# Kernel tuning notes

Hardware: AMD Instinct MI355X
Metric: run time of the kernel (lower is better)

## Reference

```python
import jax, jax.numpy as jnp
import numpy as np

N_DRUG, N_DIS = 3072, 3072
N = N_DRUG + N_DIS
E = 196608
F1, F2, F3 = 512, 256, 128
GAMMA1 = GAMMA2 = GAMMA3 = 0.03125
NEG_SLOPE = 0.2   # GATConv default negative_slope
KERNEL_W = 0.25   # drug_ps/dis_ps = 1/kernel_len


def gat_layer(x, src, dst, w_e, W, a_src, a_dst, b):
    """Single-head GATConv: gather -> per-node softmax -> scatter-aggregate.
    Edge weights w_e scale the unnormalized attention."""
    xw = x @ W                                                  # [N, F]
    e = jax.nn.leaky_relu((xw @ a_src)[src] + (xw @ a_dst)[dst], NEG_SLOPE)  # [E]
    m = jax.ops.segment_max(e, dst, num_segments=N)
    ex = jnp.exp(e - m[dst]) * w_e
    denom = jax.ops.segment_sum(ex, dst, num_segments=N)
    alpha = ex / (denom[dst] + 1e-16)
    out = jax.ops.segment_sum(alpha[:, None] * xw[src], dst, num_segments=N)
    return out + b


def gip_kernel(y, gamma):
    """getGipKernel(y, 0, gamma, normalized=True)."""
    mn = jnp.min(y, axis=1, keepdims=True)
    mx = jnp.max(y, axis=1, keepdims=True)
    y = (y - mn) / (mx - mn + 1e-12)          # row-wise min-max normalize
    k = y @ y.T
    k = k / jnp.mean(jnp.diagonal(k))
    d = jnp.diagonal(k)
    dist = d[:, None] + d[None, :] - 2.0 * k  # kernelToDistance
    return jnp.exp(-gamma * dist)


def normalized_kernel(K):
    K = jnp.abs(K)
    minv = jnp.min(jnp.where(K > 0, K, jnp.inf))
    K = jnp.where(K == 0, minv, K)            # replace zeros with min nonzero
    d = jnp.sqrt(jnp.diagonal(K))
    return K / (d[:, None] * d[None, :])


def setup_inputs() -> dict:
    key = jax.random.key(0)
    ks = jax.random.split(key, 20)
    f32 = jnp.float32

    def lin(k, fi, fo):
        return jax.random.normal(k, (fi, fo), f32) * (1.0 / float(np.sqrt(fi)))

    inp = {
        'x': jax.random.normal(ks[0], (N, N), f32),
        'edge_index': jax.random.randint(ks[1], (2, E), 0, N, dtype=jnp.int32),
        'adj_data': jax.random.uniform(ks[2], (N, N), f32),
        'drug_sim': jax.random.uniform(ks[3], (N_DRUG, N_DRUG), f32),
        'dis_sim': jax.random.uniform(ks[4], (N_DIS, N_DIS), f32),
        'alpha1': jax.random.normal(ks[5], (N_DRUG, N_DIS), f32),
        'alpha2': jax.random.normal(ks[6], (N_DIS, N_DRUG), f32),
        'W1': lin(ks[7], N, F1),
        'as1': jax.random.normal(ks[8], (F1,), f32) * 0.1,
        'ad1': jax.random.normal(ks[9], (F1,), f32) * 0.1,
        'b1': jnp.zeros((F1,), f32),
        'W2': lin(ks[10], F1, F2),
        'as2': jax.random.normal(ks[11], (F2,), f32) * 0.1,
        'ad2': jax.random.normal(ks[12], (F2,), f32) * 0.1,
        'b2': jnp.zeros((F2,), f32),
        'W3': lin(ks[13], F2, F3),
        'as3': jax.random.normal(ks[14], (F3,), f32) * 0.1,
        'ad3': jax.random.normal(ks[15], (F3,), f32) * 0.1,
        'b3': jnp.zeros((F3,), f32),
    }
    return inp


def reference(x, edge_index, adj_data, drug_sim, dis_sim, alpha1, alpha2,
              W1, as1, ad1, b1, W2, as2, ad2, b2, W3, as3, ad3, b3):
    src0, dst0 = edge_index[0], edge_index[1]
    w0 = adj_data[src0, dst0]                  # per-edge gather of dense weights
    loop = jnp.arange(N, dtype=src0.dtype)     # GATConv add_self_loops=True
    src = jnp.concatenate([src0, loop])
    dst = jnp.concatenate([dst0, loop])
    w = jnp.concatenate([w0, jnp.ones((N,), adj_data.dtype)])

    H1 = jax.nn.relu(gat_layer(x, src, dst, w, W1, as1, ad1, b1))
    H2 = jax.nn.relu(gat_layer(H1, src, dst, w, W2, as2, ad2, b2))
    H3 = jax.nn.relu(gat_layer(H2, src, dst, w, W3, as3, ad3, b3))

    drug_k = KERNEL_W * (gip_kernel(H1[:N_DRUG], GAMMA1)
                         + gip_kernel(H2[:N_DRUG], GAMMA2)
                         + gip_kernel(H3[:N_DRUG], GAMMA3) + drug_sim)
    dis_k = KERNEL_W * (gip_kernel(H1[N_DRUG:], GAMMA1)
                        + gip_kernel(H2[N_DRUG:], GAMMA2)
                        + gip_kernel(H3[N_DRUG:], GAMMA3) + dis_sim)

    out1 = normalized_kernel(drug_k) @ alpha1  # [N_DRUG, N_DIS]
    out2 = normalized_kernel(dis_k) @ alpha2   # [N_DIS, N_DRUG]
    return 0.5 * (out1 + out2.T)
```

## Files before the change

### kernel.cpp

```cpp
#include <hip/hip_runtime.h>
#include <hip/hip_bf16.h>
#include <stdint.h>

#define N_NODES 6144
#define N_DRUG  3072
#define N_EDGE  196608
#define E_TOT   (N_EDGE + N_NODES)
#define GAMMA   0.03125f

typedef __bf16 bf16x8 __attribute__((ext_vector_type(8)));
typedef float  f32x4  __attribute__((ext_vector_type(4)));

__device__ __forceinline__ unsigned short f2b(float f){
  union { float f; unsigned u; } v; v.f = f;
  unsigned r = v.u + 0x7FFFu + ((v.u >> 16) & 1u);
  return (unsigned short)(r >> 16);
}
__device__ __forceinline__ float b2f(unsigned short b){
  union { unsigned u; float f; } v; v.u = ((unsigned)b) << 16;
  return v.f;
}
__device__ __forceinline__ void gl_lds(const void* g, void* l){
  __builtin_amdgcn_global_load_lds((const __attribute__((address_space(1))) void*)g,
                                   (__attribute__((address_space(3))) void*)l, 16, 0, 0);
}

#define WAITVM(N) asm volatile("s_waitcnt vmcnt(" #N ")" ::: "memory")
#define SYNC() { __builtin_amdgcn_sched_barrier(0); __builtin_amdgcn_s_barrier(); __builtin_amdgcn_sched_barrier(0); }

__global__ void cast_bf16_k(const float* __restrict__ in, unsigned short* __restrict__ out, long n){
  long i = ((long)blockIdx.x*blockDim.x + threadIdx.x)*4;
  long stride = (long)gridDim.x*blockDim.x*4;
  for (; i < n; i += stride){
    float4 v = *(const float4*)(in + i);
    ushort4 o;
    o.x = f2b(v.x); o.y = f2b(v.y); o.z = f2b(v.z); o.w = f2b(v.w);
    *(ushort4*)(out + i) = o;
  }
}

__global__ void tcast_k(const float* __restrict__ in, unsigned short* __restrict__ out,
                        int R, int Cd, int OLD, int OOFF){
  __shared__ float tile[32][33];
  int bx = blockIdx.x*32, by = blockIdx.y*32;
  int tx = threadIdx.x, ty = threadIdx.y;
  for (int i = ty; i < 32; i += 8) tile[i][tx] = in[(long)(by+i)*Cd + bx + tx];
  __syncthreads();
  for (int i = ty; i < 32; i += 8) out[(long)(bx+i)*OLD + OOFF + by + tx] = f2b(tile[tx][i]);
}

__global__ void tcast2_k(const float* __restrict__ a2, const float* __restrict__ a1,
                         unsigned short* __restrict__ o0, unsigned short* __restrict__ o1){
  __shared__ float tile[32][33];
  const float* in = blockIdx.z ? a1 : a2;
  unsigned short* out = blockIdx.z ? o1 : o0;
  int OOFF = blockIdx.z ? 0 : N_DRUG;
  int bx = blockIdx.x*32, by = blockIdx.y*32;
  int tx = threadIdx.x, ty = threadIdx.y;
  for (int i = ty; i < 32; i += 8) tile[i][tx] = in[(long)(by+i)*N_DRUG + bx + tx];
  __syncthreads();
  for (int i = ty; i < 32; i += 8) out[(long)(bx+i)*N_NODES + OOFF + by + tx] = f2b(tile[tx][i]);
}

__global__ void hist_k(const int* __restrict__ ei, int* __restrict__ cnt){
  int i = blockIdx.x*blockDim.x + threadIdx.x;
  if (i >= E_TOT) return;
  int d = (i < N_EDGE) ? ei[N_EDGE + i] : (i - N_EDGE);
  atomicAdd(&cnt[d], 1);
}

__global__ void scan_k(const int* __restrict__ cnt, int* __restrict__ ptr){
  __shared__ int sums[1024];
  int t = threadIdx.x;
  int v[6]; int s = 0;
  #pragma unroll
  for (int i = 0; i < 6; i++){ v[i] = s; s += cnt[t*6 + i]; }
  sums[t] = s; __syncthreads();
  for (int off = 1; off < 1024; off <<= 1){
    int add = (t >= off) ? sums[t - off] : 0;
    __syncthreads();
    sums[t] += add;
    __syncthreads();
  }
  int base = (t == 0) ? 0 : sums[t-1];
  #pragma unroll
  for (int i = 0; i < 6; i++) ptr[t*6 + i] = base + v[i];
  if (t == 1023) ptr[N_NODES] = sums[1023];
}

__global__ void scatter_k(const int* __restrict__ ei, const int* __restrict__ ptr,
                          int* __restrict__ cur, int* __restrict__ srcs,
                          int* __restrict__ epos){
  int i = blockIdx.x*blockDim.x + threadIdx.x;
  if (i >= E_TOT) return;
  int s = (i < N_EDGE) ? ei[i] : (i - N_EDGE);
  int d = (i < N_EDGE) ? ei[N_EDGE + i] : (i - N_EDGE);
  int pos = ptr[d] + atomicAdd(&cur[d], 1);
  srcs[pos] = s; epos[i] = pos;
}

__global__ void dots_k(const float* __restrict__ XW, const float* __restrict__ av,
                       const float* __restrict__ dv, float* __restrict__ es,
                       float* __restrict__ ed, float* __restrict__ denom, int F){
  int n = blockIdx.x, l = threadIdx.x;
  float s = 0.f, d = 0.f;
  for (int f = l; f < F; f += 64){
    float x = XW[(long)n*F + f];
    s += x * av[f]; d += x * dv[f];
  }
  #pragma unroll
  for (int off = 32; off > 0; off >>= 1){ s += __shfl_down(s, off); d += __shfl_down(d, off); }
  if (l == 0){ es[n] = s; ed[n] = d; denom[n] = 0.f; }
}

__global__ void phase12_k(const int* __restrict__ ei, const float* __restrict__ adj,
                          const float* __restrict__ es, const float* __restrict__ ed,
                          const int* __restrict__ epos, float* __restrict__ exc,
                          float* __restrict__ denom){
  int i = blockIdx.x*blockDim.x + threadIdx.x;
  if (i >= E_TOT) return;
  int s = (i < N_EDGE) ? ei[i] : (i - N_EDGE);
  int d = (i < N_EDGE) ? ei[N_EDGE + i] : (i - N_EDGE);
  float w = (i < N_EDGE) ? adj[(long)s*N_NODES + d] : 1.0f;
  float e = es[s] + ed[d];
  e = (e > 0.f) ? e : 0.2f*e;
  float ex = expf(e) * w;
  exc[epos[i]] = ex;
  atomicAdd(&denom[d], ex);
}

__global__ void agg4_k(const unsigned short* __restrict__ XWb, const int* __restrict__ ptr,
                       const int* __restrict__ srcs, const float* __restrict__ exc,
                       const float* __restrict__ denom, const float* __restrict__ bias,
                       float* __restrict__ H, unsigned short* __restrict__ Hb, int F){
  int n = blockIdx.x, t = threadIdx.x;
  int st = ptr[n], en = ptr[n+1];
  float a0v = 0.f, a1v = 0.f, a2v = 0.f, a3v = 0.f;
  int j = st;
  for (; j + 1 < en; j += 2){
    float w0 = exc[j], w1 = exc[j+1];
    int s0 = srcs[j], s1 = srcs[j+1];
    ushort4 u0 = *(const ushort4*)(XWb + (long)s0*F + t*4);
    ushort4 u1 = *(const ushort4*)(XWb + (long)s1*F + t*4);
    a0v += w0*b2f(u0.x) + w1*b2f(u1.x); a1v += w0*b2f(u0.y) + w1*b2f(u1.y);
    a2v += w0*b2f(u0.z) + w1*b2f(u1.z); a3v += w0*b2f(u0.w) + w1*b2f(u1.w);
  }
  if (j < en){
    float w0 = exc[j]; int s0 = srcs[j];
    ushort4 u0 = *(const ushort4*)(XWb + (long)s0*F + t*4);
    a0v += w0*b2f(u0.x); a1v += w0*b2f(u0.y); a2v += w0*b2f(u0.z); a3v += w0*b2f(u0.w);
  }
  float invd = 1.f/(denom[n] + 1e-16f);
  float4 b = *(const float4*)(bias + t*4);
  float4 o;
  o.x = fmaxf(a0v*invd + b.x, 0.f); o.y = fmaxf(a1v*invd + b.y, 0.f);
  o.z = fmaxf(a2v*invd + b.z, 0.f); o.w = fmaxf(a3v*invd + b.w, 0.f);
  *(float4*)(H + (long)n*F + t*4) = o;
  if (Hb){
    ushort4 ob; ob.x = f2b(o.x); ob.y = f2b(o.y); ob.z = f2b(o.z); ob.w = f2b(o.w);
    *(ushort4*)(Hb + (long)n*F + t*4) = ob;
  }
}

__global__ void agg_k(const unsigned short* __restrict__ XWb, const int* __restrict__ ptr,
                      const int* __restrict__ srcs, const float* __restrict__ exc,
                      const float* __restrict__ denom, const float* __restrict__ bias,
                      float* __restrict__ H, unsigned short* __restrict__ Hb, int F){
  int n = blockIdx.x, t = threadIdx.x;
  int st = ptr[n], en = ptr[n+1];
  float ax = 0.f, ay = 0.f;
  int j = st;
  for (; j + 1 < en; j += 2){
    float a0 = exc[j], a1 = exc[j+1];
    int s0 = srcs[j], s1 = srcs[j+1];
    ushort2 u0 = *(const ushort2*)(XWb + (long)s0*F + t*2);
    ushort2 u1 = *(const ushort2*)(XWb + (long)s1*F + t*2);
    ax += a0*b2f(u0.x) + a1*b2f(u1.x);
    ay += a0*b2f(u0.y) + a1*b2f(u1.y);
  }
  if (j < en){
    float a = exc[j]; int s = srcs[j];
    ushort2 u = *(const ushort2*)(XWb + (long)s*F + t*2);
    ax += a*b2f(u.x); ay += a*b2f(u.y);
  }
  float invd = 1.f/(denom[n] + 1e-16f);
  float2 b = *(const float2*)(bias + t*2);
  float vx = fmaxf(ax*invd + b.x, 0.f);
  float vy = fmaxf(ay*invd + b.y, 0.f);
  *(float2*)(H + (long)n*F + t*2) = make_float2(vx, vy);
  if (Hb){
    ushort2 o; o.x = f2b(vx); o.y = f2b(vy);
    *(ushort2*)(Hb + (long)n*F + t*2) = o;
  }
}

__global__ void rownorm_all_k(const float* __restrict__ H0, const float* __restrict__ H1,
                              const float* __restrict__ H2,
                              unsigned short* __restrict__ y0, unsigned short* __restrict__ y1,
                              float* __restrict__ dv0, float* __restrict__ dv1){
  int seg = blockIdx.y;
  int side = seg / 3, layer = seg % 3;
  int F = 512 >> layer;
  const float* H = (layer == 0) ? H0 : (layer == 1) ? H1 : H2;
  H += (size_t)(side ? N_DRUG : 0) * F;
  unsigned short* yb = ((side ? y1 : y0) + ((layer == 0) ? 0 : (layer == 1) ? 512 : 768));
  float* dvec = (side ? dv1 : dv0) + layer*N_DRUG;

  int r = blockIdx.x, t = threadIdx.x;
  __shared__ float ra[256], rb[256];
  float mn = 3.4e38f, mx = -3.4e38f;
  for (int f = t; f < F; f += 256){
    float v = H[(long)r*F + f];
    mn = fminf(mn, v); mx = fmaxf(mx, v);
  }
  ra[t] = mn; rb[t] = mx; __syncthreads();
  for (int s2 = 128; s2 > 0; s2 >>= 1){
    if (t < s2){ ra[t] = fminf(ra[t], ra[t+s2]); rb[t] = fmaxf(rb[t], rb[t+s2]); }
    __syncthreads();
  }
  mn = ra[0]; mx = rb[0];
  __syncthreads();
  float sc = 1.f/(mx - mn + 1e-12f);
  float s = 0.f;
  for (int f = t; f < F; f += 256){
    float v = (H[(long)r*F + f] - mn)*sc;
    unsigned short b = f2b(v);
    yb[(long)r*896 + f] = b;
    float vb = b2f(b);
    s += vb*vb;
  }
  ra[t] = s; __syncthreads();
  for (int s2 = 128; s2 > 0; s2 >>= 1){
    if (t < s2) ra[t] += ra[t+s2];
    __syncthreads();
  }
  if (t == 0) dvec[r] = ra[0];
}

__global__ void vsum_diag_k(const float* __restrict__ dv0, const float* __restrict__ dv1,
                            float* __restrict__ sump,
                            const float* __restrict__ sim0, const float* __restrict__ sim1,
                            float* __restrict__ rs0, float* __restrict__ rs1){
  int y = blockIdx.y;
  int t = threadIdx.x;
  if (y < 6){
    int side = y / 3, layer = y % 3;
    const float* v = (side ? dv1 : dv0) + layer*N_DRUG;
    __shared__ float red[256];
    float s = 0.f;
    for (int i = blockIdx.x*256 + t; i < N_DRUG; i += gridDim.x*256) s += v[i];
    red[t] = s; __syncthreads();
    for (int s2 = 128; s2 > 0; s2 >>= 1){ if (t < s2) red[t] += red[t+s2]; __syncthreads(); }
    if (t == 0) atomicAdd(&sump[y], red[0]);
  } else {
    int side = y - 6;
    int i = blockIdx.x*256 + t;
    const float* sim = side ? sim1 : sim0;
    float* rs = side ? rs1 : rs0;
    if (i < N_DRUG) rs[i] = rsqrtf(sim[(long)i*N_DRUG + i] + 3.0f);
  }
}

__global__ __launch_bounds__(512, 2) void gemm8p(
    const unsigned short* __restrict__ A, const unsigned short* __restrict__ Bt,
    float* __restrict__ P, float* __restrict__ Palt, int M, int N, int K, int kz)
{
  __shared__ unsigned short lds[2][2][16384];
  int t = threadIdx.x;
  int lane = t & 63, wave = t >> 6;
  int wm = wave >> 2, wn = wave & 3;

  int nbx = gridDim.x;
  int nwg = nbx * gridDim.y;
  int bid = blockIdx.y * nbx + blockIdx.x;
  int cpx = nwg >> 3;
  int swz = (bid & 7) * cpx + (bid >> 3);
  long brow = (long)(swz / nbx) * 256;
  long bcol = (long)(swz % nbx) * 256;
  long k0 = (long)blockIdx.z * kz;
  int nt = kz >> 6;

  int sr = wave*8 + (lane >> 3);
  int cg = (lane & 7) ^ (lane >> 3);
  const unsigned short* gA = A  + (brow + sr)*(long)K + k0 + cg*8;
  const unsigned short* gB = Bt + (bcol + sr)*(long)K + k0 + cg*8;
  unsigned ldsw = wave * 512;

  auto stage = [&](int b, int mat, int h, int tk){
    const unsigned short* g = (mat ? gB : gA) + (long)(h*128)*K + (long)tk*64;
    unsigned short* d = &lds[b][mat][h*8192 + ldsw];
    gl_lds(g, d);
    gl_lds(g + (long)64*K, d + 4096);
  };

  int fr = lane & 15, q = lane >> 4;
  int lo = fr*64 + ((q ^ (fr & 7))*8);
  int dk = (lo ^ 32) - lo;

  f32x4 acc[8][4];
  #pragma unroll
  for (int a = 0; a < 8; a++)
    #pragma unroll
    for (int b = 0; b < 4; b++){ acc[a][b][0]=0.f; acc[a][b][1]=0.f; acc[a][b][2]=0.f; acc[a][b][3]=0.f; }
  bf16x8 af[4][2], bf[4][2];

  const unsigned short* a0p = &lds[0][0][wm*8192 + lo];
  const unsigned short* b0p = &lds[0][1][wn*4096 + lo];
  const unsigned short* a1p = &lds[1][0][wm*8192 + lo];
  const unsigned short* b1p = &lds[1][1][wn*4096 + lo];

#define RD_AF_LO(ab) { _Pragma("unroll") for (int j = 0; j < 4; ++j){ \
    af[j][0] = *(const bf16x8*)((ab) + j*1024); af[j][1] = *(const bf16x8*)((ab) + j*1024 + dk); } }
#define RD_AF_HI(ab) { _Pragma("unroll") for (int j = 0; j < 4; ++j){ \
    af[j][0] = *(const bf16x8*)((ab) + (4+j)*1024); af[j][1] = *(const bf16x8*)((ab) + (4+j)*1024 + dk); } }
#define RD_BF_LO(bb) { _Pragma("unroll") for (int j = 0; j < 2; ++j){ \
    bf[j][0] = *(const bf16x8*)((bb) + j*1024); bf[j][1] = *(const bf16x8*)((bb) + j*1024 + dk); } }
#define RD_BF_HI(bb) { _Pragma("unroll") for (int j = 2; j < 4; ++j){ \
    bf[j][0] = *(const bf16x8*)((bb) + j*1024); bf[j][1] = *(const bf16x8*)((bb) + j*1024 + dk); } }
#define MFMA_Q(MB, NB) { __builtin_amdgcn_s_setprio(1); \
    _Pragma("unroll") for (int kk = 0; kk < 2; ++kk) \
      _Pragma("unroll") for (int mi = 0; mi < 4; ++mi) \
        _Pragma("unroll") for (int ni = (NB); ni < (NB)+2; ++ni) \
          acc[(MB)+mi][ni] = __builtin_amdgcn_mfma_f32_16x16x32_bf16(af[mi][kk], bf[ni][kk], acc[(MB)+mi][ni], 0, 0, 0); \
    __builtin_amdgcn_s_setprio(0); }

  stage(0,0,0,0); stage(0,0,1,0); stage(0,1,0,0); stage(0,1,1,0);
  stage(1,1,0,1); stage(1,1,1,1);
  WAITVM(4);
  SYNC();

  int half = nt >> 1;
  for (int i = 0; i < half; ++i){
    int t1 = 2*i+1, t2 = 2*i+2, t3 = 2*i+3;
    bool s2 = t2 < nt, s3 = t3 < nt;
    RD_AF_LO(a0p); RD_BF_LO(b0p);
    stage(1,0,0,t1);
    SYNC(); MFMA_Q(0,0); SYNC();
    RD_BF_HI(b0p);
    stage(1,0,1,t1);
    SYNC(); MFMA_Q(0,2); SYNC();
    RD_AF_HI(a0p);
    if (s2) stage(0,1,0,t2);
    SYNC(); MFMA_Q(4,0); SYNC();
    if (s2){ stage(0,1,1,t2); WAITVM(4); } else { WAITVM(0); }
    SYNC(); MFMA_Q(4,2); SYNC();
    RD_AF_LO(a1p); RD_BF_LO(b1p);
    if (s2) stage(0,0,0,t2);
    SYNC(); MFMA_Q(0,0); SYNC();
    RD_BF_HI(b1p);
    if (s2) stage(0,0,1,t2);
    SYNC(); MFMA_Q(0,2); SYNC();
    RD_AF_HI(a1p);
    if (s3) stage(1,1,0,t3);
    SYNC(); MFMA_Q(4,0); SYNC();
    if (s3){ stage(1,1,1,t3); WAITVM(4); } else { WAITVM(0); }
    SYNC(); MFMA_Q(4,2); SYNC();
  }
#undef RD_AF_LO
#undef RD_AF_HI
#undef RD_BF_LO
#undef RD_BF_HI
#undef MFMA_Q

  int z = blockIdx.z;
  float* Pz = (z < 2) ? (P + (long)z*M*N) : (Palt + (long)(z-2)*M*N);
  #pragma unroll
  for (int mi = 0; mi < 8; ++mi){
    #pragma unroll
    for (int ni = 0; ni < 4; ++ni){
      long col = bcol + wn*64 + ni*16 + fr;
      #pragma unroll
      for (int r = 0; r < 4; ++r){
        long row = brow + wm*128 + mi*16 + q*4 + r;
        Pz[row*N + col] = acc[mi][ni][r];
      }
    }
  }
}

__global__ void reduce4b_k(const float* __restrict__ p, float* __restrict__ out,
                           unsigned short* __restrict__ outb, long n){
  long i = ((long)blockIdx.x*blockDim.x + threadIdx.x)*4;
  if (i >= n) return;
  float4 s = *(const float4*)(p + i);
  #pragma unroll
  for (int z = 1; z < 4; z++){
    float4 x = *(const float4*)(p + (long)z*n + i);
    s.x += x.x; s.y += x.y; s.z += x.z; s.w += x.w;
  }
  *(float4*)(out + i) = s;
  ushort4 o; o.x = f2b(s.x); o.y = f2b(s.y); o.z = f2b(s.z); o.w = f2b(s.w);
  *(ushort4*)(outb + i) = o;
}

__global__ void reduce3h_k(const float* __restrict__ pa, const float* __restrict__ pb,
                           const float* __restrict__ pc, float* __restrict__ out, long n){
  long i = ((long)blockIdx.x*blockDim.x + threadIdx.x)*4;
  if (i >= n) return;
  float4 a = *(const float4*)(pa + i);
  float4 b = *(const float4*)(pb + i);
  float4 c = *(const float4*)(pc + i);
  float4 o;
  o.x = 0.5f*(a.x + b.x + c.x); o.y = 0.5f*(a.y + b.y + c.y);
  o.z = 0.5f*(a.z + b.z + c.z); o.w = 0.5f*(a.w + b.w + c.w);
  *(float4*)(out + i) = o;
}

__global__ __launch_bounds__(256) void gemm_tn(
    const unsigned short* __restrict__ A, const unsigned short* __restrict__ Bt,
    float* __restrict__ C, unsigned short* __restrict__ Cb, int M, int N, int K)
{
  __shared__ unsigned short As[2][128*64];
  __shared__ unsigned short Bs[2][128*64];
  int t = threadIdx.x;
  int wave = t >> 6, lane = t & 63;
  int brow = blockIdx.y*128, bcol = blockIdx.x*128;
  int wr = (wave >> 1)*64, wc = (wave & 1)*64;
  int fr = lane & 15, q = lane >> 4;
  int rin = lane >> 3, kslot = (lane & 7) ^ rin;

  f32x4 acc[4][4];
  #pragma unroll
  for (int a = 0; a < 4; a++)
    #pragma unroll
    for (int b = 0; b < 4; b++){ acc[a][b][0]=0.f; acc[a][b][1]=0.f; acc[a][b][2]=0.f; acc[a][b][3]=0.f; }

  int aoff[4][2], boff[4][2];
  #pragma unroll
  for (int mi = 0; mi < 4; mi++){
    int row = wr + mi*16 + fr;
    #pragma unroll
    for (int kk = 0; kk < 2; kk++) aoff[mi][kk] = row*64 + (((kk*4 + q) ^ (row & 7))*8);
  }
  #pragma unroll
  for (int ni = 0; ni < 4; ni++){
    int row = wc + ni*16 + fr;
    #pragma unroll
    for (int kk = 0; kk < 2; kk++) boff[ni][kk] = row*64 + (((kk*4 + q) ^ (row & 7))*8);
  }

  auto stage = [&](int buf, int k0){
    #pragma unroll
    for (int p = 0; p < 4; p++){
      int rsec = p*32 + wave*8;
      gl_lds(A  + (long)(brow + rsec + rin)*K + k0 + kslot*8, &As[buf][rsec*64]);
      gl_lds(Bt + (long)(bcol + rsec + rin)*K + k0 + kslot*8, &Bs[buf][rsec*64]);
    }
  };

  int nsteps = K >> 6;
  stage(0, 0);
  __syncthreads();
  int curb = 0;
  for (int s = 0; s < nsteps; s++){
    if (s + 1 < nsteps) stage(curb ^ 1, (s + 1)*64);
    const unsigned short* a_l = As[curb];
    const unsigned short* b_l = Bs[curb];
    #pragma unroll
    for (int kk = 0; kk < 2; kk++){
      bf16x8 af[4], bfv[4];
      #pragma unroll
      for (int mi = 0; mi < 4; mi++) af[mi]  = *(const bf16x8*)(a_l + aoff[mi][kk]);
      #pragma unroll
      for (int ni = 0; ni < 4; ni++) bfv[ni] = *(const bf16x8*)(b_l + boff[ni][kk]);
      #pragma unroll
      for (int mi = 0; mi < 4; mi++)
        #pragma unroll
        for (int ni = 0; ni < 4; ni++)
          acc[mi][ni] = __builtin_amdgcn_mfma_f32_16x16x32_bf16(af[mi], bfv[ni], acc[mi][ni], 0, 0, 0);
    }
    __syncthreads();
    curb ^= 1;
  }

  #pragma unroll
  for (int mi = 0; mi < 4; mi++){
    #pragma unroll
    for (int ni = 0; ni < 4; ni++){
      int col = bcol + wc + ni*16 + fr;
      #pragma unroll
      for (int r = 0; r < 4; r++){
        int row = brow + wr + mi*16 + q*4 + r;
        long idx = (long)row*N + col;
        float v = acc[mi][ni][r];
        C[idx] = v;
        if (Cb) Cb[idx] = f2b(v);
      }
    }
  }
}

__global__ __launch_bounds__(512) void gip_gemm(
    const unsigned short* __restrict__ Y0, const unsigned short* __restrict__ Y1,
    const float* __restrict__ sim0, const float* __restrict__ sim1,
    const float* __restrict__ dva, const float* __restrict__ dvb,
    const float* __restrict__ sumps,
    const float* __restrict__ rs0, const float* __restrict__ rs1,
    unsigned short* __restrict__ o0, unsigned short* __restrict__ o1)
{
  __shared__ unsigned short As[2][128*64];
  __shared__ unsigned short Bs[2][128*64];
  const int K = 896;
  int side = blockIdx.z;
  const unsigned short* Y = side ? Y1 : Y0;
  const float* sim  = side ? sim1 : sim0;
  const float* dv   = side ? dvb : dva;
  const float* sums = sumps + side*3;
  const float* rs   = side ? rs1 : rs0;
  unsigned short* outp = side ? o1 : o0;
  int outoff = side ? N_DRUG : 0;

  int t = threadIdx.x;
  int wave = t >> 6, lane = t & 63;
  int brow = blockIdx.y*128, bcol = blockIdx.x*128;
  int wr = (wave >> 1)*32, wc = (wave & 1)*64;
  int fr = lane & 15, q = lane >> 4;
  int rin = lane >> 3, kslot = (lane & 7) ^ rin;

  f32x4 acc0[2][4], acc1[2][4], acc2[2][4];
  #pragma unroll
  for (int a = 0; a < 2; a++)
    #pragma unroll
    for (int b = 0; b < 4; b++){
      acc0[a][b][0]=0.f;acc0[a][b][1]=0.f;acc0[a][b][2]=0.f;acc0[a][b][3]=0.f;
      acc1[a][b][0]=0.f;acc1[a][b][1]=0.f;acc1[a][b][2]=0.f;acc1[a][b][3]=0.f;
      acc2[a][b][0]=0.f;acc2[a][b][1]=0.f;acc2[a][b][2]=0.f;acc2[a][b][3]=0.f;
    }

  int aoff[2][2], boff[4][2];
  #pragma unroll
  for (int mi = 0; mi < 2; mi++){
    int row = wr + mi*16 + fr;
    #pragma unroll
    for (int kk = 0; kk < 2; kk++) aoff[mi][kk] = row*64 + (((kk*4 + q) ^ (row & 7))*8);
  }
  #pragma unroll
  for (int ni = 0; ni < 4; ni++){
    int row = wc + ni*16 + fr;
    #pragma unroll
    for (int kk = 0; kk < 2; kk++) boff[ni][kk] = row*64 + (((kk*4 + q) ^ (row & 7))*8);
  }

  auto stage = [&](int buf, int k0){
    #pragma unroll
    for (int p = 0; p < 2; p++){
      int rsec = p*64 + wave*8;
      gl_lds(Y + (long)(brow + rsec + rin)*K + k0 + kslot*8, &As[buf][rsec*64]);
      gl_lds(Y + (long)(bcol + rsec + rin)*K + k0 + kslot*8, &Bs[buf][rsec*64]);
    }
  };

  int curb = 0, s = 0;
  stage(0, 0);
  __syncthreads();

#define GSTEP(ACC) { \
    if (s + 1 < 14) stage(curb ^ 1, (s + 1)*64); \
    const unsigned short* a_l = As[curb]; \
    const unsigned short* b_l = Bs[curb]; \
    _Pragma("unroll") \
    for (int kk = 0; kk < 2; kk++){ \
      bf16x8 af0 = *(const bf16x8*)(a_l + aoff[0][kk]); \
      bf16x8 af1 = *(const bf16x8*)(a_l + aoff[1][kk]); \
      _Pragma("unroll") \
      for (int ni = 0; ni < 4; ni++){ \
        bf16x8 bv = *(const bf16x8*)(b_l + boff[ni][kk]); \
        ACC[0][ni] = __builtin_amdgcn_mfma_f32_16x16x32_bf16(af0, bv, ACC[0][ni], 0, 0, 0); \
        ACC[1][ni] = __builtin_amdgcn_mfma_f32_16x16x32_bf16(af1, bv, ACC[1][ni], 0, 0, 0); \
      } \
    } \
    __syncthreads(); curb ^= 1; s++; }

  for (int i = 0; i < 8; i++) GSTEP(acc0)
  for (int i = 0; i < 4; i++) GSTEP(acc1)
  for (int i = 0; i < 2; i++) GSTEP(acc2)
#undef GSTEP

  float im0 = (float)N_DRUG / sums[0];
  float im1 = (float)N_DRUG / sums[1];
  float im2 = (float)N_DRUG / sums[2];
  #pragma unroll
  for (int mi = 0; mi < 2; mi++){
    #pragma unroll
    for (int ni = 0; ni < 4; ni++){
      int col = bcol + wc + ni*16 + fr;
      float d0c = dv[col], d1c = dv[N_DRUG + col], d2c = dv[2*N_DRUG + col];
      float rc = rs[col];
      #pragma unroll
      for (int r = 0; r < 4; r++){
        int row = brow + wr + mi*16 + q*4 + r;
        float v = sim[(long)row*N_DRUG + col]
                + expf(-GAMMA*((dv[row]            + d0c - 2.f*acc0[mi][ni][r])*im0))
                + expf(-GAMMA*((dv[N_DRUG + row]   + d1c - 2.f*acc1[mi][ni][r])*im1))
                + expf(-GAMMA*((dv[2*N_DRUG + row] + d2c - 2.f*acc2[mi][ni][r])*im2));
        outp[(long)row*N_NODES + outoff + col] = f2b(v * rs[row] * rc);
      }
    }
  }
}

extern "C" void kernel_launch(void* const* d_in, const int* in_sizes, int n_in,
                              void* d_out, int out_size, void* d_ws, size_t ws_size,
                              hipStream_t stream){
  const float* x        = (const float*)d_in[0];
  const int*   ei       = (const int*)d_in[1];
  const float* adj      = (const float*)d_in[2];
  const float* drug_sim = (const float*)d_in[3];
  const float* dis_sim  = (const float*)d_in[4];
  const float* alpha1   = (const float*)d_in[5];
  const float* alpha2   = (const float*)d_in[6];
  const float* W[3]   = {(const float*)d_in[7],  (const float*)d_in[11], (const float*)d_in[15]};
  const float* as_[3] = {(const float*)d_in[8],  (const float*)d_in[12], (const float*)d_in[16]};
  const float* ad_[3] = {(const float*)d_in[9],  (const float*)d_in[13], (const float*)d_in[17]};
  const float* bs_[3] = {(const float*)d_in[10], (const float*)d_in[14], (const float*)d_in[18]};
  float* out = (float*)d_out;
  const int Fs[3] = {512, 256, 128};

  char* p = (char*)d_ws;
  auto alloc = [&](size_t bytes)->char*{
    char* r = p; p += (bytes + 255) & ~(size_t)255; return r;
  };
  unsigned short* xb  = (unsigned short*)alloc((size_t)N_NODES*N_NODES*2);
  unsigned short* wb  = (unsigned short*)alloc((size_t)N_NODES*512*2);
  float* XW           = (float*)alloc((size_t)N_NODES*512*4);
  unsigned short* XWb = (unsigned short*)alloc((size_t)N_NODES*512*2);
  float* Hf[3];
  Hf[0] = (float*)alloc((size_t)N_NODES*512*4);
  Hf[1] = (float*)alloc((size_t)N_NODES*256*4);
  Hf[2] = (float*)alloc((size_t)N_NODES*128*4);
  unsigned short* Hb  = (unsigned short*)alloc((size_t)N_NODES*512*2);
  float* es    = (float*)alloc(N_NODES*4);
  float* edv   = (float*)alloc(N_NODES*4);
  float* denom = (float*)alloc(N_NODES*4);
  float* exc   = (float*)alloc((size_t)E_TOT*4);
  int* cntcur  = (int*)alloc((size_t)2*N_NODES*4);
  int* cnt = cntcur, *cur = cntcur + N_NODES;
  int* cptr = (int*)alloc((N_NODES+1)*4);
  int* srcs = (int*)alloc((size_t)E_TOT*4);
  int* epos = (int*)alloc((size_t)E_TOT*4);
  unsigned short* ycat[2];
  ycat[0] = (unsigned short*)alloc((size_t)N_DRUG*896*2);
  ycat[1] = (unsigned short*)alloc((size_t)N_DRUG*896*2);
  float* dvv[2];
  dvv[0] = (float*)alloc((size_t)3*N_DRUG*4);
  dvv[1] = (float*)alloc((size_t)3*N_DRUG*4);
  float* sump = (float*)alloc(256);
  float* rsv[2];
  rsv[0] = (float*)alloc(N_DRUG*4);
  rsv[1] = (float*)alloc(N_DRUG*4);
  unsigned short* Abuf  = (unsigned short*)alloc((size_t)N_DRUG*N_NODES*2);
  unsigned short* Btbuf = (unsigned short*)alloc((size_t)N_DRUG*N_NODES*2);

  float* pL1 = (float*)Abuf;
  float* pF01 = (float*)xb;
  float* pF2  = (float*)XW;
  const long MN = (long)N_DRUG*N_DRUG;

  cast_bf16_k<<<4096, 256, 0, stream>>>(x, xb, (long)N_NODES*N_NODES);
  hipMemsetAsync(cntcur, 0, (size_t)2*N_NODES*4, stream);
  hist_k<<<(E_TOT+255)/256, 256, 0, stream>>>(ei, cnt);
  scan_k<<<1, 1024, 0, stream>>>(cnt, cptr);
  scatter_k<<<(E_TOT+255)/256, 256, 0, stream>>>(ei, cptr, cur, srcs, epos);

  const unsigned short* Ain = xb;
  int Kin = N_NODES;
  for (int l = 0; l < 3; l++){
    int F = Fs[l];
    tcast_k<<<dim3(F/32, Kin/32), dim3(32,8), 0, stream>>>(W[l], wb, Kin, F, Kin, 0);
    if (l == 0){
      gemm8p<<<dim3(F/256, N_NODES/256, 4), 512, 0, stream>>>(Ain, wb, pL1, pL1 + 2*(long)N_NODES*F, N_NODES, F, Kin, Kin/4);
      reduce4b_k<<<(int)(((long)N_NODES*F/4 + 255)/256), 256, 0, stream>>>(pL1, XW, XWb, (long)N_NODES*F);
    } else {
      gemm_tn<<<dim3(F/128, N_NODES/128), 256, 0, stream>>>(Ain, wb, XW, XWb, N_NODES, F, Kin);
    }
    dots_k<<<N_NODES, 64, 0, stream>>>(XW, as_[l], ad_[l], es, edv, denom, F);
    phase12_k<<<(E_TOT+255)/256, 256, 0, stream>>>(ei, adj, es, edv, epos, exc, denom);
    unsigned short* HbOut = (l < 2) ? Hb : nullptr;
    if (F >= 256)
      agg4_k<<<N_NODES, F/4, 0, stream>>>(XWb, cptr, srcs, exc, denom, bs_[l], Hf[l], HbOut, F);
    else
      agg_k<<<N_NODES, 64, 0, stream>>>(XWb, cptr, srcs, exc, denom, bs_[l], Hf[l], HbOut, F);
    Ain = Hb; Kin = F;
  }

  hipMemsetAsync(sump, 0, 24, stream);
  rownorm_all_k<<<dim3(N_DRUG, 6), 256, 0, stream>>>(Hf[0], Hf[1], Hf[2],
                                                     ycat[0], ycat[1], dvv[0], dvv[1]);
  vsum_diag_k<<<dim3(12, 8), 256, 0, stream>>>(dvv[0], dvv[1], sump,
                                               drug_sim, dis_sim, rsv[0], rsv[1]);

  tcast2_k<<<dim3(N_DRUG/32, N_DRUG/32, 2), dim3(32,8), 0, stream>>>(alpha2, alpha1, Abuf, Btbuf);

  gip_gemm<<<dim3(N_DRUG/128, N_DRUG/128, 2), 512, 0, stream>>>(
      ycat[0], ycat[1], drug_sim, dis_sim, dvv[0], dvv[1], sump, rsv[0], rsv[1], Abuf, Btbuf);

  gemm8p<<<dim3(N_DRUG/256, N_DRUG/256, 3), 512, 0, stream>>>(Abuf, Btbuf, pF01, pF2, N_DRUG, N_DRUG, N_NODES, N_NODES/3);
  reduce3h_k<<<(int)((MN/4 + 255)/256), 256, 0, stream>>>(pF01, pF01 + MN, pF2, out, MN);

  (void)in_sizes; (void)n_in; (void)out_size; (void)ws_size;
}
```

Before: 600.0 us.

## Drop fp32 activation copies and precompute CSR-ordered edge weights once

Stops writing fp32 copies of XW and the layer outputs and keeps only the bf16 versions, which dots_k and rownorm now read. The per-edge adjacency gather moves into scatter_k, done once into CSR order together with destination indices, so phase12 reads srcs/dsts/wcsr contiguously instead of gathering adj and writing exc through epos every layer. This cuts memory traffic, at the cost of computing the attention logits and min-max normalisation from bf16-rounded values.

Measured after the change: 623.3 us. 3.9% more time.

```diff
diff --git a/kernel.cpp b/kernel.cpp
--- a/kernel.cpp
+++ b/kernel.cpp
@@ -88,24 +88,26 @@
   if (t == 1023) ptr[N_NODES] = sums[1023];
 }
 
-__global__ void scatter_k(const int* __restrict__ ei, const int* __restrict__ ptr,
-                          int* __restrict__ cur, int* __restrict__ srcs,
-                          int* __restrict__ epos){
+__global__ void scatter_k(const int* __restrict__ ei, const float* __restrict__ adj,
+                          const int* __restrict__ ptr, int* __restrict__ cur,
+                          int* __restrict__ srcs, int* __restrict__ dsts,
+                          float* __restrict__ wcsr){
   int i = blockIdx.x*blockDim.x + threadIdx.x;
   if (i >= E_TOT) return;
   int s = (i < N_EDGE) ? ei[i] : (i - N_EDGE);
   int d = (i < N_EDGE) ? ei[N_EDGE + i] : (i - N_EDGE);
   int pos = ptr[d] + atomicAdd(&cur[d], 1);
-  srcs[pos] = s; epos[i] = pos;
-}
-
-__global__ void dots_k(const float* __restrict__ XW, const float* __restrict__ av,
+  srcs[pos] = s; dsts[pos] = d;
+  wcsr[pos] = (i < N_EDGE) ? adj[(long)s*N_NODES + d] : 1.0f;
+}
+
+__global__ void dots_k(const unsigned short* __restrict__ XWb, const float* __restrict__ av,
                        const float* __restrict__ dv, float* __restrict__ es,
                        float* __restrict__ ed, float* __restrict__ denom, int F){
   int n = blockIdx.x, l = threadIdx.x;
   float s = 0.f, d = 0.f;
   for (int f = l; f < F; f += 64){
-    float x = XW[(long)n*F + f];
+    float x = b2f(XWb[(long)n*F + f]);
     s += x * av[f]; d += x * dv[f];
   }
   #pragma unroll
@@ -113,26 +115,24 @@
   if (l == 0){ es[n] = s; ed[n] = d; denom[n] = 0.f; }
 }
 
-__global__ void phase12_k(const int* __restrict__ ei, const float* __restrict__ adj,
+__global__ void phase12_k(const int* __restrict__ srcs, const int* __restrict__ dsts,
+                          const float* __restrict__ wcsr,
                           const float* __restrict__ es, const float* __restrict__ ed,
-                          const int* __restrict__ epos, float* __restrict__ exc,
-                          float* __restrict__ denom){
-  int i = blockIdx.x*blockDim.x + threadIdx.x;
-  if (i >= E_TOT) return;
-  int s = (i < N_EDGE) ? ei[i] : (i - N_EDGE);
-  int d = (i < N_EDGE) ? ei[N_EDGE + i] : (i - N_EDGE);
-  float w = (i < N_EDGE) ? adj[(long)s*N_NODES + d] : 1.0f;
+                          float* __restrict__ exc, float* __restrict__ denom){
+  int p = blockIdx.x*blockDim.x + threadIdx.x;
+  if (p >= E_TOT) return;
+  int s = srcs[p], d = dsts[p];
   float e = es[s] + ed[d];
   e = (e > 0.f) ? e : 0.2f*e;
-  float ex = expf(e) * w;
-  exc[epos[i]] = ex;
+  float ex = expf(e) * wcsr[p];
+  exc[p] = ex;
   atomicAdd(&denom[d], ex);
 }
 
 __global__ void agg4_k(const unsigned short* __restrict__ XWb, const int* __restrict__ ptr,
                        const int* __restrict__ srcs, const float* __restrict__ exc,
                        const float* __restrict__ denom, const float* __restrict__ bias,
-                       float* __restrict__ H, unsigned short* __restrict__ Hb, int F){
+                       unsigned short* __restrict__ Hb, int F){
   int n = blockIdx.x, t = threadIdx.x;
   int st = ptr[n], en = ptr[n+1];
   float a0v = 0.f, a1v = 0.f, a2v = 0.f, a3v = 0.f;
@@ -152,20 +152,16 @@
   }
   float invd = 1.f/(denom[n] + 1e-16f);
   float4 b = *(const float4*)(bias + t*4);
-  float4 o;
-  o.x = fmaxf(a0v*invd + b.x, 0.f); o.y = fmaxf(a1v*invd + b.y, 0.f);
-  o.z = fmaxf(a2v*invd + b.z, 0.f); o.w = fmaxf(a3v*invd + b.w, 0.f);
-  *(float4*)(H + (long)n*F + t*4) = o;
-  if (Hb){
-    ushort4 ob; ob.x = f2b(o.x); ob.y = f2b(o.y); ob.z = f2b(o.z); ob.w = f2b(o.w);
-    *(ushort4*)(Hb + (long)n*F + t*4) = ob;
-  }
+  ushort4 ob;
+  ob.x = f2b(fmaxf(a0v*invd + b.x, 0.f)); ob.y = f2b(fmaxf(a1v*invd + b.y, 0.f));
+  ob.z = f2b(fmaxf(a2v*invd + b.z, 0.f)); ob.w = f2b(fmaxf(a3v*invd + b.w, 0.f));
+  *(ushort4*)(Hb + (long)n*F + t*4) = ob;
 }
 
 __global__ void agg_k(const unsigned short* __restrict__ XWb, const int* __restrict__ ptr,
                       const int* __restrict__ srcs, const float* __restrict__ exc,
                       const float* __restrict__ denom, const float* __restrict__ bias,
-                      float* __restrict__ H, unsigned short* __restrict__ Hb, int F){
+                      unsigned short* __restrict__ Hb, int F){
   int n = blockIdx.x, t = threadIdx.x;
   int st = ptr[n], en = ptr[n+1];
   float ax = 0.f, ay = 0.f;
@@ -185,23 +181,20 @@
   }
   float invd = 1.f/(denom[n] + 1e-16f);
   float2 b = *(const float2*)(bias + t*2);
-  float vx = fmaxf(ax*invd + b.x, 0.f);
-  float vy = fmaxf(ay*invd + b.y, 0.f);
-  *(float2*)(H + (long)n*F + t*2) = make_float2(vx, vy);
-  if (Hb){
-    ushort2 o; o.x = f2b(vx); o.y = f2b(vy);
-    *(ushort2*)(Hb + (long)n*F + t*2) = o;
-  }
-}
-
-__global__ void rownorm_all_k(const float* __restrict__ H0, const float* __restrict__ H1,
-                              const float* __restrict__ H2,
+  ushort2 o;
+  o.x = f2b(fmaxf(ax*invd + b.x, 0.f));
+  o.y = f2b(fmaxf(ay*invd + b.y, 0.f));
+  *(ushort2*)(Hb + (long)n*F + t*2) = o;
+}
+
+__global__ void rownorm_all_k(const unsigned short* __restrict__ H0, const unsigned short* __restrict__ H1,
+                              const unsigned short* __restrict__ H2,
                               unsigned short* __restrict__ y0, unsigned short* __restrict__ y1,
                               float* __restrict__ dv0, float* __restrict__ dv1){
   int seg = blockIdx.y;
   int side = seg / 3, layer = seg % 3;
   int F = 512 >> layer;
-  const float* H = (layer == 0) ? H0 : (layer == 1) ? H1 : H2;
+  const unsigned short* H = (layer == 0) ? H0 : (layer == 1) ? H1 : H2;
   H += (size_t)(side ? N_DRUG : 0) * F;
   unsigned short* yb = ((side ? y1 : y0) + ((layer == 0) ? 0 : (layer == 1) ? 512 : 768));
   float* dvec = (side ? dv1 : dv0) + layer*N_DRUG;
@@ -210,7 +203,7 @@
   __shared__ float ra[256], rb[256];
   float mn = 3.4e38f, mx = -3.4e38f;
   for (int f = t; f < F; f += 256){
-    float v = H[(long)r*F + f];
+    float v = b2f(H[(long)r*F + f]);
     mn = fminf(mn, v); mx = fmaxf(mx, v);
   }
   ra[t] = mn; rb[t] = mx; __syncthreads();
@@ -223,7 +216,7 @@
   float sc = 1.f/(mx - mn + 1e-12f);
   float s = 0.f;
   for (int f = t; f < F; f += 256){
-    float v = (H[(long)r*F + f] - mn)*sc;
+    float v = (b2f(H[(long)r*F + f]) - mn)*sc;
     unsigned short b = f2b(v);
     yb[(long)r*896 + f] = b;
     float vb = b2f(b);
@@ -378,8 +371,7 @@
   }
 }
 
-__global__ void reduce4b_k(const float* __restrict__ p, float* __restrict__ out,
-                           unsigned short* __restrict__ outb, long n){
+__global__ void reduce4b_k(const float* __restrict__ p, unsigned short* __restrict__ outb, long n){
   long i = ((long)blockIdx.x*blockDim.x + threadIdx.x)*4;
   if (i >= n) return;
   float4 s = *(const float4*)(p + i);
@@ -388,7 +380,6 @@
     float4 x = *(const float4*)(p + (long)z*n + i);
     s.x += x.x; s.y += x.y; s.z += x.z; s.w += x.w;
   }
-  *(float4*)(out + i) = s;
   ushort4 o; o.x = f2b(s.x); o.y = f2b(s.y); o.z = f2b(s.z); o.w = f2b(s.w);
   *(ushort4*)(outb + i) = o;
 }
@@ -408,7 +399,7 @@
 
 __global__ __launch_bounds__(256) void gemm_tn(
     const unsigned short* __restrict__ A, const unsigned short* __restrict__ Bt,
-    float* __restrict__ C, unsigned short* __restrict__ Cb, int M, int N, int K)
+    unsigned short* __restrict__ Cb, int M, int N, int K)
 {
   __shared__ unsigned short As[2][128*64];
   __shared__ unsigned short Bs[2][128*64];
@@ -481,10 +472,7 @@
       #pragma unroll
       for (int r = 0; r < 4; r++){
         int row = brow + wr + mi*16 + q*4 + r;
-        long idx = (long)row*N + col;
-        float v = acc[mi][ni][r];
-        C[idx] = v;
-        if (Cb) Cb[idx] = f2b(v);
+        Cb[(long)row*N + col] = f2b(acc[mi][ni][r]);
       }
     }
   }
@@ -622,13 +610,11 @@
   };
   unsigned short* xb  = (unsigned short*)alloc((size_t)N_NODES*N_NODES*2);
   unsigned short* wb  = (unsigned short*)alloc((size_t)N_NODES*512*2);
-  float* XW           = (float*)alloc((size_t)N_NODES*512*4);
   unsigned short* XWb = (unsigned short*)alloc((size_t)N_NODES*512*2);
-  float* Hf[3];
-  Hf[0] = (float*)alloc((size_t)N_NODES*512*4);
-  Hf[1] = (float*)alloc((size_t)N_NODES*256*4);
-  Hf[2] = (float*)alloc((size_t)N_NODES*128*4);
-  unsigned short* Hb  = (unsigned short*)alloc((size_t)N_NODES*512*2);
+  unsigned short* HbL[3];
+  HbL[0] = (unsigned short*)alloc((size_t)N_NODES*512*2);
+  HbL[1] = (unsigned short*)alloc((size_t)N_NODES*256*2);
+  HbL[2] = (unsigned short*)alloc((size_t)N_NODES*128*2);
   float* es    = (float*)alloc(N_NODES*4);
   float* edv   = (float*)alloc(N_NODES*4);
   float* denom = (float*)alloc(N_NODES*4);
@@ -636,8 +622,9 @@
   int* cntcur  = (int*)alloc((size_t)2*N_NODES*4);
   int* cnt = cntcur, *cur = cntcur + N_NODES;
   int* cptr = (int*)alloc((N_NODES+1)*4);
-  int* srcs = (int*)alloc((size_t)E_TOT*4);
-  int* epos = (int*)alloc((size_t)E_TOT*4);
+  int* srcs  = (int*)alloc((size_t)E_TOT*4);
+  int* dsts  = (int*)alloc((size_t)E_TOT*4);
+  float* wcsr = (float*)alloc((size_t)E_TOT*4);
   unsigned short* ycat[2];
   ycat[0] = (unsigned short*)alloc((size_t)N_DRUG*896*2);
   ycat[1] = (unsigned short*)alloc((size_t)N_DRUG*896*2);
@@ -653,14 +640,14 @@
 
   float* pL1 = (float*)Abuf;
   float* pF01 = (float*)xb;
-  float* pF2  = (float*)XW;
+  float* pF2  = (float*)wb;
   const long MN = (long)N_DRUG*N_DRUG;
 
   cast_bf16_k<<<4096, 256, 0, stream>>>(x, xb, (long)N_NODES*N_NODES);
   hipMemsetAsync(cntcur, 0, (size_t)2*N_NODES*4, stream);
   hist_k<<<(E_TOT+255)/256, 256, 0, stream>>>(ei, cnt);
   scan_k<<<1, 1024, 0, stream>>>(cnt, cptr);
-  scatter_k<<<(E_TOT+255)/256, 256, 0, stream>>>(ei, cptr, cur, srcs, epos);
+  scatter_k<<<(E_TOT+255)/256, 256, 0, stream>>>(ei, adj, cptr, cur, srcs, dsts, wcsr);
 
   const unsigned short* Ain = xb;
   int Kin = N_NODES;
@@ -669,22 +656,21 @@
     tcast_k<<<dim3(F/32, Kin/32), dim3(32,8), 0, stream>>>(W[l], wb, Kin, F, Kin, 0);
     if (l == 0){
       gemm8p<<<dim3(F/256, N_NODES/256, 4), 512, 0, stream>>>(Ain, wb, pL1, pL1 + 2*(long)N_NODES*F, N_NODES, F, Kin, Kin/4);
-      reduce4b_k<<<(int)(((long)N_NODES*F/4 + 255)/256), 256, 0, stream>>>(pL1, XW, XWb, (long)N_NODES*F);
+      reduce4b_k<<<(int)(((long)N_NODES*F/4 + 255)/256), 256, 0, stream>>>(pL1, XWb, (long)N_NODES*F);
     } else {
-      gemm_tn<<<dim3(F/128, N_NODES/128), 256, 0, stream>>>(Ain, wb, XW, XWb, N_NODES, F, Kin);
-    }
-    dots_k<<<N_NODES, 64, 0, stream>>>(XW, as_[l], ad_[l], es, edv, denom, F);
-    phase12_k<<<(E_TOT+255)/256, 256, 0, stream>>>(ei, adj, es, edv, epos, exc, denom);
-    unsigned short* HbOut = (l < 2) ? Hb : nullptr;
+      gemm_tn<<<dim3(F/128, N_NODES/128), 256, 0, stream>>>(Ain, wb, XWb, N_NODES, F, Kin);
+    }
+    dots_k<<<N_NODES, 64, 0, stream>>>(XWb, as_[l], ad_[l], es, edv, denom, F);
+    phase12_k<<<(E_TOT+255)/256, 256, 0, stream>>>(srcs, dsts, wcsr, es, edv, exc, denom);
     if (F >= 256)
-      agg4_k<<<N_NODES, F/4, 0, stream>>>(XWb, cptr, srcs, exc, denom, bs_[l], Hf[l], HbOut, F);
+      agg4_k<<<N_NODES, F/4, 0, stream>>>(XWb, cptr, srcs, exc, denom, bs_[l], HbL[l], F);
     else
-      agg_k<<<N_NODES, 64, 0, stream>>>(XWb, cptr, srcs, exc, denom, bs_[l], Hf[l], HbOut, F);
-    Ain = Hb; Kin = F;
+      agg_k<<<N_NODES, 64, 0, stream>>>(XWb, cptr, srcs, exc, denom, bs_[l], HbL[l], F);
+    Ain = HbL[l]; Kin = F;
   }
 
   hipMemsetAsync(sump, 0, 24, stream);
-  rownorm_all_k<<<dim3(N_DRUG, 6), 256, 0, stream>>>(Hf[0], Hf[1], Hf[2],
+  rownorm_all_k<<<dim3(N_DRUG, 6), 256, 0, stream>>>(HbL[0], HbL[1], HbL[2],
                                                      ycat[0], ycat[1], dvv[0], dvv[1]);
   vsum_diag_k<<<dim3(12, 8), 256, 0, stream>>>(dvv[0], dvv[1], sump,
                                                drug_sim, dis_sim, rsv[0], rsv[1]);
```
